# Optimization experiments

Measured on AMD Instinct MI355X. Metric: run time of the kernel, lower is better.

The kernel has to match this reference:

```python
import jax, jax.numpy as jnp
import numpy as np

N_NODES = 50000
N_EDGES = 1_280_000
NODE_D = 13
EDGE_RAW_D = 1
H = 64
CONCAT_D = 2 * NODE_D + EDGE_RAW_D  # 27
NEG_SLOPE = 0.2


def _leaky(x):
    return jnp.where(x >= 0, x, NEG_SLOPE * x)


def _scatter_mean(vals, idx, num_nodes):
    # vals: [E, H]; idx: [E] int -> [num_nodes, H] mean over incident edges (0 if none)
    s = jax.ops.segment_sum(vals, idx, num_segments=num_nodes)
    cnt = jax.ops.segment_sum(jnp.ones((vals.shape[0], 1), vals.dtype), idx, num_segments=num_nodes)
    return s / jnp.maximum(cnt, 1.0)


def _conv(e, src, dst, num_nodes, w_self, b_self, w_in, w_out):
    h_self = e @ w_self + b_self
    agg_in = _scatter_mean(e, dst, num_nodes)[src]   # incoming-edge mean at src nodes
    agg_out = _scatter_mean(e, src, num_nodes)[dst]  # outgoing-edge mean at dst nodes
    return _leaky(h_self + agg_in @ w_in + agg_out @ w_out)


def setup_inputs() -> dict:
    key = jax.random.key(0)
    ks = jax.random.split(key, 24)

    def lin(k, fan_in, fan_out):
        return jax.random.normal(k, (fan_in, fan_out), jnp.float32) / np.sqrt(fan_in)

    inp = {
        'x': jax.random.normal(ks[0], (N_NODES, NODE_D), jnp.float32),
        'edge_index': jax.random.randint(ks[1], (2, N_EDGES), 0, N_NODES, jnp.int32),
        'raw_edge_attr': jax.random.normal(ks[2], (N_EDGES, EDGE_RAW_D), jnp.float32),
        'enc_w': lin(ks[3], CONCAT_D, H),
        'enc_b': jnp.zeros((H,), jnp.float32),
    }
    for i, base in zip((1, 2, 3), (4, 8, 12)):
        inp[f'w_self{i}'] = lin(ks[base], H, H)
        inp[f'b_self{i}'] = jnp.zeros((H,), jnp.float32)
        inp[f'w_in{i}'] = lin(ks[base + 1], H, H)
        inp[f'w_out{i}'] = lin(ks[base + 2], H, H)
    dims = [(H, 64), (64, 64), (64, 32), (32, 1)]
    for j, (fi, fo) in enumerate(dims, start=1):
        inp[f'mlp_w{j}'] = lin(ks[15 + j], fi, fo)
        inp[f'mlp_b{j}'] = jnp.zeros((fo,), jnp.float32)
    return inp


def reference(x, edge_index, raw_edge_attr, enc_w, enc_b,
              w_self1, b_self1, w_in1, w_out1,
              w_self2, b_self2, w_in2, w_out2,
              w_self3, b_self3, w_in3, w_out3,
              mlp_w1, mlp_b1, mlp_w2, mlp_b2, mlp_w3, mlp_b3, mlp_w4, mlp_b4):
    num_nodes = x.shape[0]
    src, dst = edge_index[0], edge_index[1]
    edge_attr = jnp.concatenate([x[src], x[dst], raw_edge_attr], axis=-1)  # [E, 27]
    h = _leaky(edge_attr @ enc_w + enc_b)
    h = _conv(h, src, dst, num_nodes, w_self1, b_self1, w_in1, w_out1)
    h = _conv(h, src, dst, num_nodes, w_self2, b_self2, w_in2, w_out2)
    h = _conv(h, src, dst, num_nodes, w_self3, b_self3, w_in3, w_out3)
    h = _leaky(h @ mlp_w1 + mlp_b1)
    h = _leaky(h @ mlp_w2 + mlp_b2)
    h = _leaky(h @ mlp_w3 + mlp_b3)
    return (h @ mlp_w4 + mlp_b4).squeeze(-1)  # [E]
```

## Files before the change

### kernel.cpp

```cpp
#include <hip/hip_runtime.h>


#define NN 50000
#define NNP 50048
#define NE 1280000
#define LDP 72
#define NB 196
#define NTILES 782
#define CAP 64

#define WAVES 2
#define EDGE_ITERS 5
#define EDGE_BLOCKS 2000
#define ENC_ITERS 5
#define ENC_BLOCKS 2000

typedef unsigned int   u32;
typedef unsigned short u16;
typedef __attribute__((ext_vector_type(8))) short  short8;
typedef __attribute__((ext_vector_type(4))) float  floatx4;

#define MFMA16(a, b, c) __builtin_amdgcn_mfma_f32_16x16x32_bf16(a, b, c, 0, 0, 0)

__device__ __forceinline__ float lrelu(float x) { return fmaxf(x, 0.2f * x); }
__device__ __forceinline__ float bf2f(u16 u) { return __uint_as_float(((u32)u) << 16); }
__device__ __forceinline__ u16 f2bf(float f) {
    u32 b = __float_as_uint(f);
    return (u16)((b + 0x7FFFu + ((b >> 16) & 1u)) >> 16);
}
__device__ __forceinline__ u32 f2bf2(float lo, float hi) {
    u32 r;
    asm("v_cvt_pk_bf16_f32 %0, %1, %2" : "=v"(r) : "v"(lo), "v"(hi));
    return r;
}
__device__ __forceinline__ void ub2(u32 w, float& lo, float& hi) {
    lo = __uint_as_float(w << 16);
    hi = __uint_as_float(w & 0xFFFF0000u);
}

__device__ __forceinline__ short8 bfragP(const float* __restrict__ W, int ld, int n, int k0) {
    short8 b;
#pragma unroll
    for (int j = 0; j < 8; ++j) {
        const int p = k0 + j;
        const int k = (p & 3) * 16 + (p >> 2);
        b[j] = (short)f2bf(W[k * ld + n]);
    }
    return b;
}

__device__ __forceinline__ void mm_tile(const u16* __restrict__ tb,
                                        const short8 wf[2][4],
                                        floatx4 acc[4][4], int c16, int q4) {
#pragma unroll
    for (int mt = 0; mt < 4; ++mt) {
        const short8 a0 = *(const short8*)(tb + (mt * 16 + c16) * LDP + q4 * 8);
        const short8 a1 = *(const short8*)(tb + (mt * 16 + c16) * LDP + 32 + q4 * 8);
#pragma unroll
        for (int nt = 0; nt < 4; ++nt) {
            acc[mt][nt] = MFMA16(a0, wf[0][nt], acc[mt][nt]);
            acc[mt][nt] = MFMA16(a1, wf[1][nt], acc[mt][nt]);
        }
    }
}

__global__ void __launch_bounds__(256)
k_prep(const float* __restrict__ x, u16* __restrict__ xb)
{
    const int n = blockIdx.x * 256 + threadIdx.x;
    if (n >= NN) return;
    float f[13];
#pragma unroll
    for (int j = 0; j < 13; ++j) f[j] = x[n * 13 + j];
    uint4 p0, p1;
    p0.x = f2bf2(f[0],  f[1]);  p0.y = f2bf2(f[2],  f[3]);
    p0.z = f2bf2(f[4],  f[5]);  p0.w = f2bf2(f[6],  f[7]);
    p1.x = f2bf2(f[8],  f[9]);  p1.y = f2bf2(f[10], f[11]);
    p1.z = f2bf2(f[12], 0.0f);  p1.w = 0u;
    *(uint4*)(xb + (size_t)n * 16)     = p0;
    *(uint4*)(xb + (size_t)n * 16 + 8) = p1;
}

__global__ void __launch_bounds__(128)
k_enc(const u16* __restrict__ xb, const int* __restrict__ ei,
      const float* __restrict__ raw, const float* __restrict__ wenc,
      const float* __restrict__ benc, u16* __restrict__ hm,
      int* __restrict__ cnt_in, int* __restrict__ cnt_out,
      int* __restrict__ csr_in, int* __restrict__ csr_out)
{
    __shared__ int sidx[WAVES][64], didx[WAVES][64];
    const int w = threadIdx.x >> 6, lane = threadIdx.x & 63;
    const int c16 = lane & 15, q4 = lane >> 4;

    short8 wf[4];
    float bias[4];
#pragma unroll
    for (int nt = 0; nt < 4; ++nt) {
        short8 b;
#pragma unroll
        for (int j = 0; j < 8; ++j) {
            const int p = q4 * 8 + j;
            int row;
            if (p < 13)                 row = p;
            else if (p == 13)           row = 26;
            else if (p >= 16 && p < 29) row = 13 + (p - 16);
            else                        row = -1;
            b[j] = (short)(row >= 0 ? f2bf(wenc[row * 64 + nt * 16 + c16]) : 0);
        }
        wf[nt] = b;
        bias[nt] = benc[nt * 16 + c16];
    }

    for (int it = 0; it < ENC_ITERS; ++it) {
        const int tileId = (it * ENC_BLOCKS + blockIdx.x) * WAVES + w;
        const int e0 = tileId * 64;

        const int ms = ei[e0 + lane];
        const int md = ei[NE + e0 + lane];
        sidx[w][lane] = ms;
        didx[w][lane] = md;

        const int eidx = e0 + lane;
        const int p = atomicAdd(&cnt_out[ms], 1);
        if (p < CAP) csr_out[ms * CAP + p] = eidx;
        const int q = atomicAdd(&cnt_in[md], 1);
        if (q < CAP) csr_in[md * CAP + q] = eidx;

#pragma unroll
        for (int mt = 0; mt < 4; ++mt) {
            const int arow = mt * 16 + c16;
            const int* nbase = (q4 < 2) ? sidx[w] : didx[w];
            const int node = nbase[arow];
            short8 a = *(const short8*)(xb + (size_t)node * 16 + (q4 & 1) * 8);
            const float rv = raw[e0 + arow];
            if (q4 == 1) a[5] = (short)(u16)f2bf2(rv, 0.0f);

            floatx4 acc[4];
#pragma unroll
            for (int nt = 0; nt < 4; ++nt) acc[nt] = (floatx4)(0.0f);
#pragma unroll
            for (int nt = 0; nt < 4; ++nt) acc[nt] = MFMA16(a, wf[nt], acc[nt]);
#pragma unroll
            for (int r = 0; r < 4; ++r) {
                const int rowi = mt * 16 + q4 * 4 + r;
                uint2 pkt;
                pkt.x = f2bf2(lrelu(acc[0][r] + bias[0]), lrelu(acc[1][r] + bias[1]));
                pkt.y = f2bf2(lrelu(acc[2][r] + bias[2]), lrelu(acc[3][r] + bias[3]));
                *(uint2*)(hm + (size_t)(e0 + rowi) * 64 + c16 * 4) = pkt;
            }
        }
    }
}

__global__ void __launch_bounds__(256)
k_mean(const u16* __restrict__ hm,
       const int* __restrict__ cnt_in, const int* __restrict__ csr_in,
       const int* __restrict__ cnt_out, const int* __restrict__ csr_out,
       u16* __restrict__ m_in, u16* __restrict__ m_out)
{
    const int w = threadIdx.x >> 6, lane = threadIdx.x & 63;
    const int node = blockIdx.x * 4 + w;
    const int rg = lane >> 3;
    const int co = (lane & 7) * 8;

    for (int pass = 0; pass < 2; ++pass) {
        const int* cnt = pass ? cnt_out : cnt_in;
        const int* csr = pass ? csr_out : csr_in;
        u16* mp        = pass ? m_out : m_in;

        const int deg = min(cnt[node], CAP);
        const int b0 = node * CAP, b1 = b0 + deg;
        float fa[8], fb[8];
#pragma unroll
        for (int c = 0; c < 8; ++c) { fa[c] = 0.f; fb[c] = 0.f; }

        int j = b0;
        for (; j + 16 <= b1; j += 16) {
            const int ea = csr[j + rg];
            const int eb = csr[j + 8 + rg];
            const uint4 va = *(const uint4*)(hm + (size_t)ea * 64 + co);
            const uint4 vb = *(const uint4*)(hm + (size_t)eb * 64 + co);
            float l0, h0, l1, h1, l2, h2, l3, h3;
            ub2(va.x, l0, h0); ub2(va.y, l1, h1); ub2(va.z, l2, h2); ub2(va.w, l3, h3);
            fa[0] += l0; fa[1] += h0; fa[2] += l1; fa[3] += h1;
            fa[4] += l2; fa[5] += h2; fa[6] += l3; fa[7] += h3;
            ub2(vb.x, l0, h0); ub2(vb.y, l1, h1); ub2(vb.z, l2, h2); ub2(vb.w, l3, h3);
            fb[0] += l0; fb[1] += h0; fb[2] += l1; fb[3] += h1;
            fb[4] += l2; fb[5] += h2; fb[6] += l3; fb[7] += h3;
        }
        for (; j < b1; j += 8) {
            const int jj = j + rg;
            const int idx = jj < b1 ? jj : b0;
            const float fl = jj < b1 ? 1.f : 0.f;
            const int e = csr[idx];
            const uint4 v = *(const uint4*)(hm + (size_t)e * 64 + co);
            float l0, h0, l1, h1, l2, h2, l3, h3;
            ub2(v.x, l0, h0); ub2(v.y, l1, h1); ub2(v.z, l2, h2); ub2(v.w, l3, h3);
            fa[0] += fl * l0; fa[1] += fl * h0; fa[2] += fl * l1; fa[3] += fl * h1;
            fa[4] += fl * l2; fa[5] += fl * h2; fa[6] += fl * l3; fa[7] += fl * h3;
        }
#pragma unroll
        for (int c = 0; c < 8; ++c) fa[c] += fb[c];
#pragma unroll
        for (int d = 8; d < 64; d <<= 1)
#pragma unroll
            for (int c = 0; c < 8; ++c) fa[c] += __shfl_xor(fa[c], d, 64);

        const float inv = 1.0f / (float)(deg > 0 ? deg : 1);
        if (lane < 8) {
            uint4 p;
            p.x = f2bf2(fa[0] * inv, fa[1] * inv);
            p.y = f2bf2(fa[2] * inv, fa[3] * inv);
            p.z = f2bf2(fa[4] * inv, fa[5] * inv);
            p.w = f2bf2(fa[6] * inv, fa[7] * inv);
            *(uint4*)(mp + (size_t)node * 64 + lane * 8) = p;
        }
    }
}

__global__ void __launch_bounds__(256)
k_nodemm(u16* t_in, u16* t_out,
         const float* __restrict__ w_in, const float* __restrict__ w_out)
{
    const int w = threadIdx.x >> 6, lane = threadIdx.x & 63;
    const int c16 = lane & 15, q4 = lane >> 4;
    const int tileId = blockIdx.x * 4 + w;
    if (tileId >= NTILES) return;
    const int n0 = tileId * 64;

    for (int pass = 0; pass < 2; ++pass) {
        u16* tp         = pass ? t_out : t_in;
        const float* wp = pass ? w_out : w_in;

        short8 wf[2][4];
#pragma unroll
        for (int ks = 0; ks < 2; ++ks)
#pragma unroll
            for (int nt = 0; nt < 4; ++nt)
                wf[ks][nt] = bfragP(wp, 64, nt * 16 + c16, ks * 32 + q4 * 8);

#pragma unroll
        for (int mt = 0; mt < 4; ++mt) {
            const short8* ap = (const short8*)(tp + (size_t)(n0 + mt * 16 + c16) * 64 + q4 * 8);
            const short8 a0 = ap[0];
            const short8 a1 = ap[4];
            floatx4 acc[4];
#pragma unroll
            for (int nt = 0; nt < 4; ++nt) acc[nt] = (floatx4)(0.0f);
#pragma unroll
            for (int nt = 0; nt < 4; ++nt) {
                acc[nt] = MFMA16(a0, wf[0][nt], acc[nt]);
                acc[nt] = MFMA16(a1, wf[1][nt], acc[nt]);
            }
#pragma unroll
            for (int r = 0; r < 4; ++r) {
                const int node = n0 + mt * 16 + q4 * 4 + r;
                if (node < NN) {
                    uint2 pkt;
                    pkt.x = f2bf2(acc[0][r], acc[1][r]);
                    pkt.y = f2bf2(acc[2][r], acc[3][r]);
                    *(uint2*)(tp + (size_t)node * 64 + c16 * 4) = pkt;
                }
            }
        }
    }
}

__global__ void __launch_bounds__(128, 4)
k_edge(const float* __restrict__ wself, const float* __restrict__ bself,
       const u16* __restrict__ t_in, const u16* __restrict__ t_out,
       const int* __restrict__ ei, u16* __restrict__ hm)
{
    __shared__ int sidx[WAVES][64], didx[WAVES][64];
    const int w = threadIdx.x >> 6, lane = threadIdx.x & 63;
    const int c16 = lane & 15, q4 = lane >> 4;

    short8 wf[2][4];
    float bias[4];
#pragma unroll
    for (int ks = 0; ks < 2; ++ks)
#pragma unroll
        for (int nt = 0; nt < 4; ++nt)
            wf[ks][nt] = bfragP(wself, 64, nt * 16 + c16, ks * 32 + q4 * 8);
#pragma unroll
    for (int nt = 0; nt < 4; ++nt) bias[nt] = bself[nt * 16 + c16];

    for (int it = 0; it < EDGE_ITERS; ++it) {
        const int tileId = (it * EDGE_BLOCKS + blockIdx.x) * WAVES + w;
        const int e0 = tileId * 64;
        sidx[w][lane] = ei[e0 + lane];
        didx[w][lane] = ei[NE + e0 + lane];

#pragma unroll
        for (int mt = 0; mt < 4; ++mt) {
            const short8* ap = (const short8*)(hm + (size_t)(e0 + mt * 16 + c16) * 64 + q4 * 8);
            const short8 a0 = ap[0];
            const short8 a1 = ap[4];
            floatx4 acc[4];
#pragma unroll
            for (int nt = 0; nt < 4; ++nt) acc[nt] = (floatx4)(0.0f);
#pragma unroll
            for (int nt = 0; nt < 4; ++nt) {
                acc[nt] = MFMA16(a0, wf[0][nt], acc[nt]);
                acc[nt] = MFMA16(a1, wf[1][nt], acc[nt]);
            }
            float tv[4][4], uv[4][4];
#pragma unroll
            for (int r = 0; r < 4; ++r) {
                const int s = sidx[w][mt * 16 + q4 * 4 + r];
                const uint2 v = *(const uint2*)(t_in + (size_t)s * 64 + c16 * 4);
                ub2(v.x, tv[r][0], tv[r][1]); ub2(v.y, tv[r][2], tv[r][3]);
            }
#pragma unroll
            for (int r = 0; r < 4; ++r) {
                const int d = didx[w][mt * 16 + q4 * 4 + r];
                const uint2 v = *(const uint2*)(t_out + (size_t)d * 64 + c16 * 4);
                ub2(v.x, uv[r][0], uv[r][1]); ub2(v.y, uv[r][2], uv[r][3]);
            }
#pragma unroll
            for (int r = 0; r < 4; ++r) {
                const int row = mt * 16 + q4 * 4 + r;
                const float v0 = lrelu(acc[0][r] + bias[0] + tv[r][0] + uv[r][0]);
                const float v1 = lrelu(acc[1][r] + bias[1] + tv[r][1] + uv[r][1]);
                const float v2 = lrelu(acc[2][r] + bias[2] + tv[r][2] + uv[r][2]);
                const float v3 = lrelu(acc[3][r] + bias[3] + tv[r][3] + uv[r][3]);
                uint2 pkt; pkt.x = f2bf2(v0, v1); pkt.y = f2bf2(v2, v3);
                *(uint2*)(hm + (size_t)(e0 + row) * 64 + c16 * 4) = pkt;
            }
        }
    }
}

__global__ void __launch_bounds__(128, 2)
k_edge_mlp(const float* __restrict__ wself, const float* __restrict__ bself,
           const u16* __restrict__ t_in, const u16* __restrict__ t_out,
           const int* __restrict__ ei, const u16* __restrict__ hm,
           const float* __restrict__ w1, const float* __restrict__ b1,
           const float* __restrict__ w2, const float* __restrict__ b2,
           const float* __restrict__ w3, const float* __restrict__ b3,
           const float* __restrict__ w4, const float* __restrict__ b4,
           float* __restrict__ out)
{
    __shared__ alignas(16) u16 tile[WAVES][64 * LDP];
    __shared__ int sidx[WAVES][64], didx[WAVES][64];
    const int w = threadIdx.x >> 6, lane = threadIdx.x & 63;
    const int c16 = lane & 15, q4 = lane >> 4;

    short8 wfS[2][4], wf1[2][4], wf2[2][4], wf3[2][2];
    float bS[4], bv1[4], bv2[4], bv3[2];
#pragma unroll
    for (int ks = 0; ks < 2; ++ks) {
#pragma unroll
        for (int nt = 0; nt < 4; ++nt) {
            wfS[ks][nt] = bfragP(wself, 64, nt * 16 + c16, ks * 32 + q4 * 8);
            wf1[ks][nt] = bfragP(w1,    64, nt * 16 + c16, ks * 32 + q4 * 8);
            wf2[ks][nt] = bfragP(w2,    64, nt * 16 + c16, ks * 32 + q4 * 8);
        }
#pragma unroll
        for (int nt = 0; nt < 2; ++nt)
            wf3[ks][nt] = bfragP(w3, 32, nt * 16 + c16, ks * 32 + q4 * 8);
    }
#pragma unroll
    for (int nt = 0; nt < 4; ++nt) { bS[nt] = bself[nt*16+c16]; bv1[nt] = b1[nt*16+c16]; bv2[nt] = b2[nt*16+c16]; }
#pragma unroll
    for (int nt = 0; nt < 2; ++nt) bv3[nt] = b3[nt * 16 + c16];
    const float w4a = w4[c16], w4b = w4[16 + c16], b4v = b4[0];

    for (int it = 0; it < EDGE_ITERS; ++it) {
        const int tileId = (it * EDGE_BLOCKS + blockIdx.x) * WAVES + w;
        const int e0 = tileId * 64;
        sidx[w][lane] = ei[e0 + lane];
        didx[w][lane] = ei[NE + e0 + lane];

#pragma unroll
        for (int mt = 0; mt < 4; ++mt) {
            const short8* ap = (const short8*)(hm + (size_t)(e0 + mt * 16 + c16) * 64 + q4 * 8);
            const short8 a0 = ap[0];
            const short8 a1 = ap[4];
            floatx4 acc[4];
#pragma unroll
            for (int nt = 0; nt < 4; ++nt) acc[nt] = (floatx4)(0.0f);
#pragma unroll
            for (int nt = 0; nt < 4; ++nt) {
                acc[nt] = MFMA16(a0, wfS[0][nt], acc[nt]);
                acc[nt] = MFMA16(a1, wfS[1][nt], acc[nt]);
            }
            float tv[4][4], uv[4][4];
#pragma unroll
            for (int r = 0; r < 4; ++r) {
                const int s = sidx[w][mt * 16 + q4 * 4 + r];
                const uint2 v = *(const uint2*)(t_in + (size_t)s * 64 + c16 * 4);
                ub2(v.x, tv[r][0], tv[r][1]); ub2(v.y, tv[r][2], tv[r][3]);
            }
#pragma unroll
            for (int r = 0; r < 4; ++r) {
                const int d = didx[w][mt * 16 + q4 * 4 + r];
                const uint2 v = *(const uint2*)(t_out + (size_t)d * 64 + c16 * 4);
                ub2(v.x, uv[r][0], uv[r][1]); ub2(v.y, uv[r][2], uv[r][3]);
            }
#pragma unroll
            for (int r = 0; r < 4; ++r) {
                const int row = mt * 16 + q4 * 4 + r;
                const float v0 = lrelu(acc[0][r] + bS[0] + tv[r][0] + uv[r][0]);
                const float v1 = lrelu(acc[1][r] + bS[1] + tv[r][1] + uv[r][1]);
                const float v2 = lrelu(acc[2][r] + bS[2] + tv[r][2] + uv[r][2]);
                const float v3 = lrelu(acc[3][r] + bS[3] + tv[r][3] + uv[r][3]);
                uint2 pkt; pkt.x = f2bf2(v0, v1); pkt.y = f2bf2(v2, v3);
                *(uint2*)(tile[w] + row * LDP + c16 * 4) = pkt;
            }
        }

        floatx4 acc[4][4];
#pragma unroll
        for (int mt = 0; mt < 4; ++mt)
#pragma unroll
            for (int nt = 0; nt < 4; ++nt) acc[mt][nt] = (floatx4)(0.0f);
        mm_tile(tile[w], wf1, acc, c16, q4);
#pragma unroll
        for (int mt = 0; mt < 4; ++mt)
#pragma unroll
            for (int r = 0; r < 4; ++r) {
                const int row = mt * 16 + q4 * 4 + r;
                uint2 pkt;
                pkt.x = f2bf2(lrelu(acc[mt][0][r] + bv1[0]), lrelu(acc[mt][1][r] + bv1[1]));
                pkt.y = f2bf2(lrelu(acc[mt][2][r] + bv1[2]), lrelu(acc[mt][3][r] + bv1[3]));
                *(uint2*)(tile[w] + row * LDP + c16 * 4) = pkt;
            }

#pragma unroll
        for (int mt = 0; mt < 4; ++mt)
#pragma unroll
            for (int nt = 0; nt < 4; ++nt) acc[mt][nt] = (floatx4)(0.0f);
        mm_tile(tile[w], wf2, acc, c16, q4);
#pragma unroll
        for (int mt = 0; mt < 4; ++mt)
#pragma unroll
            for (int r = 0; r < 4; ++r) {
                const int row = mt * 16 + q4 * 4 + r;
                uint2 pkt;
                pkt.x = f2bf2(lrelu(acc[mt][0][r] + bv2[0]), lrelu(acc[mt][1][r] + bv2[1]));
                pkt.y = f2bf2(lrelu(acc[mt][2][r] + bv2[2]), lrelu(acc[mt][3][r] + bv2[3]));
                *(uint2*)(tile[w] + row * LDP + c16 * 4) = pkt;
            }

        floatx4 a3[4][2];
#pragma unroll
        for (int mt = 0; mt < 4; ++mt)
#pragma unroll
            for (int nt = 0; nt < 2; ++nt) a3[mt][nt] = (floatx4)(0.0f);
#pragma unroll
        for (int mt = 0; mt < 4; ++mt) {
            const short8 a0 = *(const short8*)(tile[w] + (mt * 16 + c16) * LDP + q4 * 8);
            const short8 a1 = *(const short8*)(tile[w] + (mt * 16 + c16) * LDP + 32 + q4 * 8);
#pragma unroll
            for (int nt = 0; nt < 2; ++nt) {
                a3[mt][nt] = MFMA16(a0, wf3[0][nt], a3[mt][nt]);
                a3[mt][nt] = MFMA16(a1, wf3[1][nt], a3[mt][nt]);
            }
        }
#pragma unroll
        for (int mt = 0; mt < 4; ++mt)
#pragma unroll
            for (int r = 0; r < 4; ++r) {
                float p = lrelu(a3[mt][0][r] + bv3[0]) * w4a
                        + lrelu(a3[mt][1][r] + bv3[1]) * w4b;
                p += __shfl_xor(p, 1, 64);
                p += __shfl_xor(p, 2, 64);
                p += __shfl_xor(p, 4, 64);
                p += __shfl_xor(p, 8, 64);
                if (c16 == 0) out[e0 + mt * 16 + q4 * 4 + r] = p + b4v;
            }
    }
}

extern "C" void kernel_launch(void* const* d_in, const int* in_sizes, int n_in,
                              void* d_out, int out_size, void* d_ws, size_t ws_size,
                              hipStream_t stream)
{
    const float* x      = (const float*)d_in[0];
    const int*   ei     = (const int*)  d_in[1];
    const float* raw    = (const float*)d_in[2];
    const float* wenc   = (const float*)d_in[3];
    const float* benc   = (const float*)d_in[4];
    const float* wself1 = (const float*)d_in[5];
    const float* bself1 = (const float*)d_in[6];
    const float* win1   = (const float*)d_in[7];
    const float* wout1  = (const float*)d_in[8];
    const float* wself2 = (const float*)d_in[9];
    const float* bself2 = (const float*)d_in[10];
    const float* win2   = (const float*)d_in[11];
    const float* wout2  = (const float*)d_in[12];
    const float* wself3 = (const float*)d_in[13];
    const float* bself3 = (const float*)d_in[14];
    const float* win3   = (const float*)d_in[15];
    const float* wout3  = (const float*)d_in[16];
    const float* w1 = (const float*)d_in[17]; const float* b1 = (const float*)d_in[18];
    const float* w2 = (const float*)d_in[19]; const float* b2 = (const float*)d_in[20];
    const float* w3 = (const float*)d_in[21]; const float* b3 = (const float*)d_in[22];
    const float* w4 = (const float*)d_in[23]; const float* b4 = (const float*)d_in[24];

    u16*   t_in    = (u16*)d_ws;
    u16*   t_out   = t_in + (size_t)NNP * 64;
    int*   cnt_in  = (int*)(t_out + (size_t)NNP * 64);
    int*   cnt_out = cnt_in + NN;
    int*   csr_in  = cnt_out + NN;
    int*   csr_out = csr_in + (size_t)NN * CAP;
    u16*   hm      = (u16*)(csr_out + (size_t)NN * CAP);

    u16*   xb      = t_in;

    hipMemsetAsync(cnt_in, 0, (size_t)2 * NN * sizeof(int), stream);

    k_prep<<<NB, 256, 0, stream>>>(x, xb);

    k_enc<<<ENC_BLOCKS, 128, 0, stream>>>(xb, ei, raw, wenc, benc, hm,
                                          cnt_in, cnt_out, csr_in, csr_out);

    for (int layer = 0; layer < 3; ++layer) {
        const float* wi = layer == 0 ? win1  : layer == 1 ? win2  : win3;
        const float* wo = layer == 0 ? wout1 : layer == 1 ? wout2 : wout3;
        k_mean<<<NN / 4, 256, 0, stream>>>(hm, cnt_in, csr_in, cnt_out, csr_out,
                                           t_in, t_out);
        k_nodemm<<<NB, 256, 0, stream>>>(t_in, t_out, wi, wo);
        if (layer == 0)
            k_edge<<<EDGE_BLOCKS, 128, 0, stream>>>(wself1, bself1, t_in, t_out, ei, hm);
        else if (layer == 1)
            k_edge<<<EDGE_BLOCKS, 128, 0, stream>>>(wself2, bself2, t_in, t_out, ei, hm);
        else
            k_edge_mlp<<<EDGE_BLOCKS, 128, 0, stream>>>(wself3, bself3, t_in, t_out, ei, hm,
                                                        w1, b1, w2, b2, w3, b3, w4, b4,
                                                        (float*)d_out);
    }
}
```

Measured before the change: 762.5 us.

## Prefetch next tile's edge features and indices in edge conv kernels

Adds software prefetching in k_edge and k_edge_mlp. Each iteration issues the next tile's hm A-fragments and src/dst indices while the current tile's MFMAs and gathers run, to hide global load latency. Grid and iteration counts also change (2500 blocks x 4 iterations), and k_edge's occupancy hint drops from 4 to 3 to make room for the extra registers. The risk is higher register pressure and lower occupancy, which could offset the latency hiding.

```diff
diff --git a/kernel.cpp b/kernel.cpp
--- a/kernel.cpp
+++ b/kernel.cpp
@@ -10,10 +10,10 @@
 #define CAP 64
 
 #define WAVES 2
-#define EDGE_ITERS 5
-#define EDGE_BLOCKS 2000
-#define ENC_ITERS 5
-#define ENC_BLOCKS 2000
+#define EDGE_ITERS 4
+#define EDGE_BLOCKS 2500
+#define ENC_ITERS 4
+#define ENC_BLOCKS 2500
 
 typedef unsigned int   u32;
 typedef unsigned short u16;
@@ -266,7 +266,7 @@
     }
 }
 
-__global__ void __launch_bounds__(128, 4)
+__global__ void __launch_bounds__(128, 3)
 k_edge(const float* __restrict__ wself, const float* __restrict__ bself,
        const u16* __restrict__ t_in, const u16* __restrict__ t_out,
        const int* __restrict__ ei, u16* __restrict__ hm)
@@ -285,24 +285,36 @@
 #pragma unroll
     for (int nt = 0; nt < 4; ++nt) bias[nt] = bself[nt * 16 + c16];
 
+    int e0 = (blockIdx.x * WAVES + w) * 64;
+    sidx[w][lane] = ei[e0 + lane];
+    didx[w][lane] = ei[NE + e0 + lane];
+    short8 pa0[4], pa1[4];
+#pragma unroll
+    for (int mt = 0; mt < 4; ++mt) {
+        const short8* ap = (const short8*)(hm + (size_t)(e0 + mt * 16 + c16) * 64 + q4 * 8);
+        pa0[mt] = ap[0]; pa1[mt] = ap[4];
+    }
+
+#pragma unroll 1
     for (int it = 0; it < EDGE_ITERS; ++it) {
-        const int tileId = (it * EDGE_BLOCKS + blockIdx.x) * WAVES + w;
-        const int e0 = tileId * 64;
-        sidx[w][lane] = ei[e0 + lane];
-        didx[w][lane] = ei[NE + e0 + lane];
+        const bool more = (it + 1 < EDGE_ITERS);
+        const int e0n = (((it + 1) * EDGE_BLOCKS + blockIdx.x) * WAVES + w) * 64;
+        int sN = 0, dN = 0;
+        if (more) { sN = ei[e0n + lane]; dN = ei[NE + e0n + lane]; }
 
 #pragma unroll
         for (int mt = 0; mt < 4; ++mt) {
-            const short8* ap = (const short8*)(hm + (size_t)(e0 + mt * 16 + c16) * 64 + q4 * 8);
-            const short8 a0 = ap[0];
-            const short8 a1 = ap[4];
             floatx4 acc[4];
 #pragma unroll
             for (int nt = 0; nt < 4; ++nt) acc[nt] = (floatx4)(0.0f);
 #pragma unroll
             for (int nt = 0; nt < 4; ++nt) {
-                acc[nt] = MFMA16(a0, wf[0][nt], acc[nt]);
-                acc[nt] = MFMA16(a1, wf[1][nt], acc[nt]);
+                acc[nt] = MFMA16(pa0[mt], wf[0][nt], acc[nt]);
+                acc[nt] = MFMA16(pa1[mt], wf[1][nt], acc[nt]);
+            }
+            if (more) {
+                const short8* ap = (const short8*)(hm + (size_t)(e0n + mt * 16 + c16) * 64 + q4 * 8);
+                pa0[mt] = ap[0]; pa1[mt] = ap[4];
             }
             float tv[4][4], uv[4][4];
 #pragma unroll
@@ -328,6 +340,8 @@
                 *(uint2*)(hm + (size_t)(e0 + row) * 64 + c16 * 4) = pkt;
             }
         }
+        if (more) { sidx[w][lane] = sN; didx[w][lane] = dN; }
+        e0 = e0n;
     }
 }
 
@@ -366,24 +380,36 @@
     for (int nt = 0; nt < 2; ++nt) bv3[nt] = b3[nt * 16 + c16];
     const float w4a = w4[c16], w4b = w4[16 + c16], b4v = b4[0];
 
+    int e0 = (blockIdx.x * WAVES + w) * 64;
+    sidx[w][lane] = ei[e0 + lane];
+    didx[w][lane] = ei[NE + e0 + lane];
+    short8 pa0[4], pa1[4];
+#pragma unroll
+    for (int mt = 0; mt < 4; ++mt) {
+        const short8* ap = (const short8*)(hm + (size_t)(e0 + mt * 16 + c16) * 64 + q4 * 8);
+        pa0[mt] = ap[0]; pa1[mt] = ap[4];
+    }
+
+#pragma unroll 1
     for (int it = 0; it < EDGE_ITERS; ++it) {
-        const int tileId = (it * EDGE_BLOCKS + blockIdx.x) * WAVES + w;
-        const int e0 = tileId * 64;
-        sidx[w][lane] = ei[e0 + lane];
-        didx[w][lane] = ei[NE + e0 + lane];
+        const bool more = (it + 1 < EDGE_ITERS);
+        const int e0n = (((it + 1) * EDGE_BLOCKS + blockIdx.x) * WAVES + w) * 64;
+        int sN = 0, dN = 0;
+        if (more) { sN = ei[e0n + lane]; dN = ei[NE + e0n + lane]; }
 
 #pragma unroll
         for (int mt = 0; mt < 4; ++mt) {
-            const short8* ap = (const short8*)(hm + (size_t)(e0 + mt * 16 + c16) * 64 + q4 * 8);
-            const short8 a0 = ap[0];
-            const short8 a1 = ap[4];
             floatx4 acc[4];
 #pragma unroll
             for (int nt = 0; nt < 4; ++nt) acc[nt] = (floatx4)(0.0f);
 #pragma unroll
             for (int nt = 0; nt < 4; ++nt) {
-                acc[nt] = MFMA16(a0, wfS[0][nt], acc[nt]);
-                acc[nt] = MFMA16(a1, wfS[1][nt], acc[nt]);
+                acc[nt] = MFMA16(pa0[mt], wfS[0][nt], acc[nt]);
+                acc[nt] = MFMA16(pa1[mt], wfS[1][nt], acc[nt]);
+            }
+            if (more) {
+                const short8* ap = (const short8*)(hm + (size_t)(e0n + mt * 16 + c16) * 64 + q4 * 8);
+                pa0[mt] = ap[0]; pa1[mt] = ap[4];
             }
             float tv[4][4], uv[4][4];
 #pragma unroll
@@ -409,6 +435,7 @@
                 *(uint2*)(tile[w] + row * LDP + c16 * 4) = pkt;
             }
         }
+        if (more) { sidx[w][lane] = sN; didx[w][lane] = dN; }
 
         floatx4 acc[4][4];
 #pragma unroll
@@ -470,6 +497,7 @@
                 p += __shfl_xor(p, 8, 64);
                 if (c16 == 0) out[e0 + mt * 16 + q4 * 4 + r] = p + b4v;
             }
+        e0 = e0n;
     }
 }
 
```

New measurement: 745.8 us. 1.02x faster.
